# Performance work log

Hardware: AMD Instinct MI355X
Metric: run time of the kernel (lower is better)

## Reference

```python
import math
import jax, jax.numpy as jnp
from jax import lax
import numpy as np

B, SEQ, D_MODEL = 8, 1024, 512
R, K, H = 3, 3, 4
DE, DH, DU, DTR, DCONV, DEMB = 64, 64, 32, 4, 3, 10


def setup_inputs() -> dict:
    key = jax.random.key(0)
    ks = iter(jax.random.split(key, 48))
    def nrm(shape, s=0.05):
        return jax.random.normal(next(ks), shape, jnp.float32) * s
    inp = {}
    inp['x'] = jax.random.normal(next(ks), (B, SEQ, D_MODEL), jnp.float32)
    # Mamba params, leading dims (R, 2) = (layer, fwd/bwd direction)
    inp['m_in_w'] = nrm((R, 2, D_MODEL, 2 * DE))
    inp['m_conv_w'] = nrm((R, 2, DE, DCONV), 0.2)
    inp['m_conv_b'] = nrm((R, 2, DE), 0.1)
    inp['m_xproj_w'] = nrm((R, 2, DE, DTR + 2 * DH))
    inp['m_dt_w'] = nrm((R, 2, DTR, DE), 0.2)
    inp['m_dt_b'] = nrm((R, 2, DE), 0.1)
    inp['m_Alog'] = jnp.broadcast_to(jnp.log(jnp.arange(1, DH + 1, dtype=jnp.float32)), (R, 2, DE, DH)) + jnp.zeros((R, 2, DE, DH), jnp.float32)
    inp['m_D'] = jnp.ones((R, 2, DE), jnp.float32)
    inp['m_out_w'] = nrm((R, 2, DE, D_MODEL))
    # LayerNorm / FFN params per layer
    inp['ln1_g'] = jnp.ones((R, D_MODEL), jnp.float32)
    inp['ln1_b'] = jnp.zeros((R, D_MODEL), jnp.float32)
    inp['ffn_w1'] = nrm((R, D_MODEL, DU))
    inp['ffn_b1'] = jnp.zeros((R, DU), jnp.float32)
    inp['ffn_w2'] = nrm((R, DU, D_MODEL))
    inp['ffn_b2'] = jnp.zeros((R, D_MODEL), jnp.float32)
    inp['ln2_g'] = jnp.ones((R, D_MODEL), jnp.float32)
    inp['ln2_b'] = jnp.zeros((R, D_MODEL), jnp.float32)
    # MAGAC params (N = D_MODEL nodes, in_dim = SEQ)
    inp['psi_emb'] = jax.random.normal(next(ks), (D_MODEL, DEMB), jnp.float32)
    inp['psi'] = jnp.array(1.0, jnp.float32)
    inp['W_q'] = jax.random.normal(next(ks), (DEMB, H, DEMB), jnp.float32)
    inp['W_k'] = jax.random.normal(next(ks), (DEMB, H, DEMB), jnp.float32)
    inp['attn_alpha'] = jnp.array(0.5, jnp.float32)
    inp['F_w'] = nrm((H, DEMB, K + 1, SEQ))
    inp['f_b'] = jax.random.normal(next(ks), (H, DEMB), jnp.float32)
    inp['head_mix'] = jnp.ones((H,), jnp.float32)
    inp['head_w'] = nrm((D_MODEL,))
    inp['head_b'] = jnp.zeros((), jnp.float32)
    return inp


def _layernorm(x, g, b, eps=1e-5):
    mu = x.mean(-1, keepdims=True)
    v = ((x - mu) ** 2).mean(-1, keepdims=True)
    return (x - mu) / jnp.sqrt(v + eps) * g + b


def _mamba(x, in_w, conv_w, conv_b, xproj_w, dt_w, dt_b, Alog, Dp, out_w):
    b, l, _ = x.shape
    xr = x @ in_w                              # (b,l,2*DE)
    xp, res = jnp.split(xr, 2, axis=-1)
    # depthwise causal conv (torch pads k-1 both sides then truncates to l == left-pad k-1)
    xc = xp.transpose(0, 2, 1)                 # (b,DE,l)
    xc = lax.conv_general_dilated(xc, conv_w[:, None, :], (1,), [(DCONV - 1, 0)],
                                  feature_group_count=DE,
                                  dimension_numbers=('NCH', 'OIH', 'NCH'))
    xc = xc + conv_b[None, :, None]
    xp = jax.nn.silu(xc.transpose(0, 2, 1))    # (b,l,DE)
    A = -jnp.exp(Alog)                         # (DE,DH)
    x_dbl = xp @ xproj_w                       # (b,l,DTR+2*DH)
    delta = jax.nn.softplus(x_dbl[..., :DTR] @ dt_w + dt_b)   # (b,l,DE)
    Bm = x_dbl[..., DTR:DTR + DH]
    Cm = x_dbl[..., DTR + DH:]
    dA = jnp.exp(delta[..., None] * A)                         # (b,l,DE,DH)
    dBu = delta[..., None] * Bm[:, :, None, :] * xp[..., None] # (b,l,DE,DH)
    def step(s, inp):
        dAt, dBt, ct = inp
        s = dAt * s + dBt
        return s, jnp.einsum('bdn,bn->bd', s, ct)
    s0 = jnp.zeros((b, DE, DH), x.dtype)
    _, ys = lax.scan(step, s0, (dA.transpose(1, 0, 2, 3), dBu.transpose(1, 0, 2, 3), Cm.transpose(1, 0, 2)))
    y = ys.transpose(1, 0, 2) + xp * Dp
    y = y * jax.nn.sigmoid(res)
    return y @ out_w


def _magac(xg, psi_emb, psi, W_q, W_k, attn_alpha, F_w, f_b, head_mix):
    # xg: (B, N, L); eval-mode deterministic path
    diff = psi_emb[:, None, :] - psi_emb[None, :, :]
    A_base = jax.nn.softmax(jnp.exp(-psi * (diff ** 2).sum(-1)), axis=1)   # (N,N)
    Q = jnp.einsum('nd,dhm->nhm', psi_emb, W_q)
    Kq = jnp.einsum('nd,dhm->nhm', psi_emb, W_k)
    attn = jax.nn.softmax(jnp.einsum('nhd,mhd->hnm', Q, Kq) / math.sqrt(DEMB), axis=-1)
    alpha = jax.nn.sigmoid(attn_alpha)
    A_eff = alpha * A_base[None] + (1.0 - alpha) * attn                    # (H,N,N)
    N = psi_emb.shape[0]
    I = jnp.broadcast_to(jnp.eye(N, dtype=xg.dtype), (H, N, N))
    sup = [I, A_eff]
    for _ in range(K - 1):
        sup.append(2.0 * jnp.matmul(A_eff, sup[-1]) - sup[-2])             # Chebyshev
    sup = jnp.stack(sup, axis=1)                                           # (H,K+1,N,N)
    Wf = jnp.einsum('nd,hdkl->hnkl', psi_emb, F_w)                         # (H,N,K+1,L)
    bf = jnp.einsum('nd,hd->hn', psi_emb, f_b)                             # (H,N)
    x_g = jnp.einsum('hknm,bml->bhknl', sup, xg)                           # (B,H,K+1,N,L)
    out_h = jnp.einsum('bhknl,hnkl->bhn', x_g, Wf) + bf[None]
    mix = jax.nn.softmax(head_mix)
    return jnp.einsum('bhn,h->bn', out_h, mix)


def reference(x, m_in_w, m_conv_w, m_conv_b, m_xproj_w, m_dt_w, m_dt_b, m_Alog, m_D, m_out_w,
              ln1_g, ln1_b, ffn_w1, ffn_b1, ffn_w2, ffn_b2, ln2_g, ln2_b,
              psi_emb, psi, W_q, W_k, attn_alpha, F_w, f_b, head_mix, head_w, head_b):
    for i in range(R):
        mf = (m_in_w[i, 0], m_conv_w[i, 0], m_conv_b[i, 0], m_xproj_w[i, 0], m_dt_w[i, 0],
              m_dt_b[i, 0], m_Alog[i, 0], m_D[i, 0], m_out_w[i, 0])
        mb = (m_in_w[i, 1], m_conv_w[i, 1], m_conv_b[i, 1], m_xproj_w[i, 1], m_dt_w[i, 1],
              m_dt_b[i, 1], m_Alog[i, 1], m_D[i, 1], m_out_w[i, 1])
        y_f = _mamba(x, *mf)
        y_b = jnp.flip(_mamba(jnp.flip(x, 1), *mb), 1)
        y = _layernorm(x + y_f + y_b, ln1_g[i], ln1_b[i])
        z = jax.nn.relu(y @ ffn_w1[i] + ffn_b1[i]) @ ffn_w2[i] + ffn_b2[i]
        x = _layernorm(y + z, ln2_g[i], ln2_b[i])
    g = _magac(x.transpose(0, 2, 1), psi_emb, psi, W_q, W_k, attn_alpha, F_w, f_b, head_mix)
    # eval-mode Bayesian MC: all mc_eval samples identical -> mean=g, var=1e-6
    log_var_node = jnp.full_like(g, jnp.log(jnp.asarray(1e-6, g.dtype)))
    mu = g @ head_w + head_b
    var = jnp.exp(log_var_node) @ (head_w ** 2) + 1e-6
    return mu, jnp.log(var)
```

## Files before the change

### kernel.cpp

```cpp
#include <hip/hip_runtime.h>
#include <math.h>

#define SEQL 1024
#define NB 8
#define DMOD 512

__device__ __forceinline__ float blk_sum4(float v, volatile float* sb) {
#pragma unroll
  for (int off = 32; off; off >>= 1) v += __shfl_xor(v, off, 64);
  int lid = threadIdx.x & 63, wid = threadIdx.x >> 6;
  if (lid == 0) sb[wid] = v;
  __syncthreads();
  float t = sb[0] + sb[1] + sb[2] + sb[3];
  __syncthreads();
  return t;
}
__device__ __forceinline__ float blk_max4(float v, volatile float* sb) {
#pragma unroll
  for (int off = 32; off; off >>= 1) v = fmaxf(v, __shfl_xor(v, off, 64));
  int lid = threadIdx.x & 63, wid = threadIdx.x >> 6;
  if (lid == 0) sb[wid] = v;
  __syncthreads();
  float t = fmaxf(fmaxf(sb[0], sb[1]), fmaxf(sb[2], sb[3]));
  __syncthreads();
  return t;
}

__global__ __launch_bounds__(256) void gemm_f32(
    const float* __restrict__ A, long aStr,
    const float* __restrict__ B, long bStr,
    const float* __restrict__ Dm, long dStr,
    float* __restrict__ C, long cStr, long cChunkStr,
    int M, int N, int K, int lda, int ldb, int ldd, int ldc,
    float alpha, float beta, int kchunks) {
  __shared__ float As[2][16][68];
  __shared__ float Bs[2][16][64];
  const int zz = blockIdx.z;
  const int zb = zz / kchunks, kc = zz % kchunks;
  A += (long)zb * aStr + (long)kc * K;
  B += (long)zb * bStr + (long)kc * K * ldb;
  Dm += (long)zb * dStr;
  C += (long)zb * cStr + (long)kc * cChunkStr;
  const int tid = threadIdx.x;
  const int m0 = blockIdx.y * 64, n0 = blockIdx.x * 64;
  const int tx = tid & 15, ty = tid >> 4;
  const int arow = tid >> 2, acol = (tid & 3) << 2;
  const int brow = tid >> 4, bcol = (tid & 15) << 2;
  const bool aOk = (m0 + arow < M);
  const float* Aptr = A + (long)(m0 + arow) * lda + acol;
  const float* Bptr = B + (long)brow * ldb;
  const int bc = n0 + bcol;
  const int kIters = K >> 4;
  float acc[4][4] = {};

  auto loadB = [&](int it) {
    const float* Bk = Bptr + (long)it * 16 * ldb;
    float4 r;
    if (bc + 3 < N) r = *(const float4*)(Bk + bc);
    else {
      r.x = (bc + 0 < N) ? Bk[bc + 0] : 0.f;
      r.y = (bc + 1 < N) ? Bk[bc + 1] : 0.f;
      r.z = (bc + 2 < N) ? Bk[bc + 2] : 0.f;
      r.w = (bc + 3 < N) ? Bk[bc + 3] : 0.f;
    }
    return r;
  };

  float4 av = make_float4(0.f, 0.f, 0.f, 0.f);
  if (aOk) av = *(const float4*)(Aptr);
  float4 bv = loadB(0);
  As[0][acol + 0][arow] = av.x; As[0][acol + 1][arow] = av.y;
  As[0][acol + 2][arow] = av.z; As[0][acol + 3][arow] = av.w;
  *(float4*)&Bs[0][brow][bcol] = bv;

  for (int it = 0; it < kIters; ++it) {
    const int cur = it & 1;
    __syncthreads();
    const bool more = (it + 1 < kIters);
    if (more) {
      if (aOk) av = *(const float4*)(Aptr + (it + 1) * 16);
      bv = loadB(it + 1);
    }
#pragma unroll
    for (int kk = 0; kk < 16; ++kk) {
      float4 aq = *(const float4*)&As[cur][kk][ty << 2];
      float4 bq = *(const float4*)&Bs[cur][kk][tx << 2];
      float aa[4] = {aq.x, aq.y, aq.z, aq.w};
      float bb[4] = {bq.x, bq.y, bq.z, bq.w};
#pragma unroll
      for (int i = 0; i < 4; ++i)
#pragma unroll
        for (int j = 0; j < 4; ++j) acc[i][j] = fmaf(aa[i], bb[j], acc[i][j]);
    }
    if (more) {
      const int nxt = cur ^ 1;
      As[nxt][acol + 0][arow] = av.x; As[nxt][acol + 1][arow] = av.y;
      As[nxt][acol + 2][arow] = av.z; As[nxt][acol + 3][arow] = av.w;
      *(float4*)&Bs[nxt][brow][bcol] = bv;
    }
  }
#pragma unroll
  for (int i = 0; i < 4; ++i) {
    int row = m0 + (ty << 2) + i;
    if (row >= M) continue;
#pragma unroll
    for (int j = 0; j < 4; ++j) {
      int col = n0 + (tx << 2) + j;
      if (col >= N) continue;
      float v = alpha * acc[i][j];
      if (beta != 0.f) v += beta * Dm[(long)row * ldd + col];
      C[(long)row * ldc + col] = v;
    }
  }
}

__global__ __launch_bounds__(256) void convproj(
    const float* __restrict__ xr, const float* __restrict__ cw,
    const float* __restrict__ cb, const float* __restrict__ pw,
    const float* __restrict__ dw, const float* __restrict__ db,
    float* __restrict__ Bm, float* __restrict__ Cm,
    float* __restrict__ xpT, float* __restrict__ dlT, float* __restrict__ sigT) {
  int dir = blockIdx.y;
  int L = blockIdx.x;
  int r = L & 7, q = L >> 3;
  int blk = r * 256 + q;
  int wv = threadIdx.x >> 6, e = threadIdx.x & 63;
  int tok = blk * 4 + wv;
  int b = tok >> 10, t = tok & 1023;
  const float* xrp = xr + (long)dir * 1048576;
  long rb = (long)tok * 128;
  const float* w = cw + dir * 192;
  float w0 = w[e * 3 + 0], w1 = w[e * 3 + 1], w2 = w[e * 3 + 2];
  float acc = cb[dir * 64 + e] + w2 * xrp[rb + e];
  if (dir == 0) {
    if (t >= 1) acc += w1 * xrp[rb - 128 + e];
    if (t >= 2) acc += w0 * xrp[rb - 256 + e];
  } else {
    if (t <= 1022) acc += w1 * xrp[rb + 128 + e];
    if (t <= 1021) acc += w0 * xrp[rb + 256 + e];
  }
  float xpv = acc / (1.f + __expf(-acc));
  float res = xrp[rb + 64 + e];
  float sg = 1.f / (1.f + __expf(-res));
  long tidx = (long)dir * 524288 + (long)b * 65536 + (long)e * 1024 + t;
  xpT[tidx] = xpv;
  sigT[tidx] = sg;
  const float* wp = pw + dir * 8448;
  float aB = 0.f, aC = 0.f, aD = 0.f;
#pragma unroll
  for (int k = 0; k < 64; ++k) {
    float xk = __shfl(xpv, k, 64);
    const float* wr = wp + k * 132;
    aB = fmaf(xk, wr[4 + e], aB);
    aC = fmaf(xk, wr[68 + e], aC);
    aD = fmaf(xk, wr[e & 3], aD);
  }
  long ob = (long)dir * 524288 + (long)tok * 64;
  Bm[ob + e] = aB;
  Cm[ob + e] = aC;
  const float* dwp = dw + dir * 256;
  float dv = db[dir * 64 + e];
#pragma unroll
  for (int rr = 0; rr < 4; ++rr) dv = fmaf(__shfl(aD, rr, 64), dwp[rr * 64 + e], dv);
  dlT[tidx] = fmaxf(dv, 0.f) + log1pf(__expf(-fabsf(dv)));
}

__device__ __forceinline__ void remap16w(int wv, int& d, int& b, int& dir, int& c) {
  int L = blockIdx.x + 64 * (blockIdx.y + 8 * blockIdx.z);
  int r = L & 7, q = L >> 3;
  d = q & 63;
  int U = (q >> 6) * 8 + r;
  int cq = U & 3;
  dir = (U >> 2) & 1;
  b = U >> 3;
  c = cq * 4 + wv;
}

__global__ __launch_bounds__(256) void scan_p1(
    const float* __restrict__ dlT, const float* __restrict__ xpT,
    const float* __restrict__ Bm, const float* __restrict__ Alog,
    float* __restrict__ Aprod, float* __restrict__ Send) {
  int wv = threadIdx.x >> 6, n = threadIdx.x & 63;
  int d, b, dir, c;
  remap16w(wv, d, b, dir, c);
  long tbase = (long)dir * 524288 + (long)b * 65536 + (long)d * 1024;
  int t0 = c * 64;
  float dl, u;
  if (dir == 0) {
    dl = dlT[tbase + t0 + n];
    u = xpT[tbase + t0 + n] * dl;
  } else {
    dl = dlT[tbase + 1023 - t0 - n];
    u = xpT[tbase + 1023 - t0 - n] * dl;
  }
  float a_dn = -__expf(Alog[dir * 4096 + d * 64 + n]);
  int tg0 = dir ? (1023 - t0) : t0;
  long bstep = dir ? -64 : 64;
  const float* bp = Bm + (long)dir * 524288 + ((long)b * 1024 + tg0) * 64 + n;
  float s = 0.f, ap = 1.f;
#pragma unroll
  for (int st = 0; st < 64; ++st) {
    float bt = *bp; bp += bstep;
    float dlv = __shfl(dl, st, 64);
    float uu = __shfl(u, st, 64);
    float a = __expf(dlv * a_dn);
    ap *= a;
    s = fmaf(a, s, uu * bt);
  }
  long sidx = ((long)((dir * 8 + b) * 64 + d)) * 1024 + c * 64 + n;
  Aprod[sidx] = ap;
  Send[sidx] = s;
}

__global__ __launch_bounds__(64) void scan_p2(
    const float* __restrict__ Aprod, const float* __restrict__ Send,
    float* __restrict__ Sin) {
  int d = blockIdx.x, b = blockIdx.y, dir = blockIdx.z;
  int n = threadIdx.x;
  long base = ((long)((dir * 8 + b) * 64 + d)) * 1024;
  float s = 0.f;
#pragma unroll
  for (int c = 0; c < 16; ++c) {
    Sin[base + c * 64 + n] = s;
    s = fmaf(Aprod[base + c * 64 + n], s, Send[base + c * 64 + n]);
  }
}

__global__ __launch_bounds__(256) void scan_p3(
    const float* __restrict__ dlT, const float* __restrict__ xpT,
    const float* __restrict__ sigT, const float* __restrict__ Bm,
    const float* __restrict__ Cm, const float* __restrict__ Alog,
    const float* __restrict__ Dp, const float* __restrict__ Sin,
    float* __restrict__ ycat) {
  __shared__ float sP[4][16 * 65];
  int wv = threadIdx.x >> 6, n = threadIdx.x & 63;
  int d, b, dir, c;
  remap16w(wv, d, b, dir, c);
  long tbase = (long)dir * 524288 + (long)b * 65536 + (long)d * 1024;
  int t0 = c * 64;
  float dl, xp, sg;
  if (dir == 0) {
    dl = dlT[tbase + t0 + n];
    xp = xpT[tbase + t0 + n];
    sg = sigT[tbase + t0 + n];
  } else {
    dl = dlT[tbase + 1023 - t0 - n];
    xp = xpT[tbase + 1023 - t0 - n];
    sg = sigT[tbase + 1023 - t0 - n];
  }
  float u = xp * dl;
  float a_dn = -__expf(Alog[dir * 4096 + d * 64 + n]);
  float dpd = Dp[dir * 64 + d];
  int tg0 = dir ? (1023 - t0) : t0;
  long bstep = dir ? -64 : 64;
  long boff = (long)dir * 524288 + ((long)b * 1024 + tg0) * 64 + n;
  const float* bp = Bm + boff;
  const float* cp = Cm + boff;
  long sidx = ((long)((dir * 8 + b) * 64 + d)) * 1024 + c * 64 + n;
  float s = Sin[sidx];
  int r4 = n >> 2, q4 = n & 3;
  for (int ph = 0; ph < 4; ++ph) {
#pragma unroll
    for (int k = 0; k < 16; ++k) {
      int st = ph * 16 + k;
      float bt = *bp; bp += bstep;
      float ct = *cp; cp += bstep;
      float dlv = __shfl(dl, st, 64);
      float uu = __shfl(u, st, 64);
      float a = __expf(dlv * a_dn);
      s = fmaf(a, s, uu * bt);
      sP[wv][k * 65 + n] = s * ct;
    }
    __syncthreads();
    float p = 0.f;
#pragma unroll
    for (int k = 0; k < 16; ++k) p += sP[wv][r4 * 65 + q4 * 16 + k];
    p += __shfl_xor(p, 1, 64);
    p += __shfl_xor(p, 2, 64);
    int stl = ph * 16 + r4;
    float xpv_r = __shfl(xp, stl, 64);
    float sgv = __shfl(sg, stl, 64);
    if (q4 == 0) {
      int tl = t0 + stl;
      int tg = dir ? 1023 - tl : tl;
      ycat[((long)b * 1024 + tg) * 128 + dir * 64 + d] = (p + xpv_r * dpd) * sgv;
    }
    __syncthreads();
  }
}

__global__ __launch_bounds__(256) void ln_ffn_ln(
    float* __restrict__ x, const float* __restrict__ g1, const float* __restrict__ b1v,
    const float* __restrict__ w1, const float* __restrict__ bb1,
    const float* __restrict__ w2, const float* __restrict__ bb2,
    const float* __restrict__ g2, const float* __restrict__ b2v) {
  __shared__ float ybuf[2][512];
  __shared__ float rbuf[2][256];
  __shared__ float zbuf[2][32];
  __shared__ float red4[16];
  int tid = threadIdx.x;
  int lid = tid & 63, wid = tid >> 6;
  float* row0 = x + (long)blockIdx.x * 1024;
  float* row1 = row0 + 512;
  float a0 = row0[tid], b0 = row0[tid + 256];
  float a1 = row1[tid], b1 = row1[tid + 256];
  float s0 = a0 + b0, q0 = a0 * a0 + b0 * b0;
  float s1 = a1 + b1, q1 = a1 * a1 + b1 * b1;
#pragma unroll
  for (int off = 32; off; off >>= 1) {
    s0 += __shfl_xor(s0, off, 64); q0 += __shfl_xor(q0, off, 64);
    s1 += __shfl_xor(s1, off, 64); q1 += __shfl_xor(q1, off, 64);
  }
  if (lid == 0) {
    red4[wid * 4 + 0] = s0; red4[wid * 4 + 1] = q0;
    red4[wid * 4 + 2] = s1; red4[wid * 4 + 3] = q1;
  }
  __syncthreads();
  float S0 = red4[0] + red4[4] + red4[8] + red4[12];
  float Q0 = red4[1] + red4[5] + red4[9] + red4[13];
  float S1 = red4[2] + red4[6] + red4[10] + red4[14];
  float Q1 = red4[3] + red4[7] + red4[11] + red4[15];
  float mu0 = S0 * (1.f / 512.f), mu1 = S1 * (1.f / 512.f);
  float r0 = 1.f / sqrtf(Q0 * (1.f / 512.f) - mu0 * mu0 + 1e-5f);
  float r1 = 1.f / sqrtf(Q1 * (1.f / 512.f) - mu1 * mu1 + 1e-5f);
  float g1a = g1[tid], g1b = g1[tid + 256];
  float b1a = b1v[tid], b1b = b1v[tid + 256];
  float y0a = (a0 - mu0) * r0 * g1a + b1a;
  float y0b = (b0 - mu0) * r0 * g1b + b1b;
  float y1a = (a1 - mu1) * r1 * g1a + b1a;
  float y1b = (b1 - mu1) * r1 * g1b + b1b;
  ybuf[0][tid] = y0a; ybuf[0][tid + 256] = y0b;
  ybuf[1][tid] = y1a; ybuf[1][tid + 256] = y1b;
  __syncthreads();
  int u = tid & 31, seg = tid >> 5;
  int k0 = seg * 64;
  float p0 = 0.f, p1 = 0.f;
#pragma unroll
  for (int k = 0; k < 64; k += 4) {
    float4 ya = *(const float4*)&ybuf[0][k0 + k];
    float4 yb = *(const float4*)&ybuf[1][k0 + k];
    float w1v0 = w1[(k0 + k + 0) * 32 + u];
    float w1v1 = w1[(k0 + k + 1) * 32 + u];
    float w1v2 = w1[(k0 + k + 2) * 32 + u];
    float w1v3 = w1[(k0 + k + 3) * 32 + u];
    p0 = fmaf(ya.w, w1v3, fmaf(ya.z, w1v2, fmaf(ya.y, w1v1, fmaf(ya.x, w1v0, p0))));
    p1 = fmaf(yb.w, w1v3, fmaf(yb.z, w1v2, fmaf(yb.y, w1v1, fmaf(yb.x, w1v0, p1))));
  }
  rbuf[0][seg * 32 + u] = p0;
  rbuf[1][seg * 32 + u] = p1;
  __syncthreads();
  if (tid < 64) {
    int t = tid >> 5, uu = tid & 31;
    float zv = bb1[uu];
#pragma unroll
    for (int sg = 0; sg < 8; ++sg) zv += rbuf[t][sg * 32 + uu];
    zbuf[t][uu] = fmaxf(zv, 0.f);
  }
  __syncthreads();
  float bb2a = bb2[tid], bb2b = bb2[tid + 256];
  float h0a = y0a + bb2a, h0b = y0b + bb2b;
  float h1a = y1a + bb2a, h1b = y1b + bb2b;
#pragma unroll
  for (int uu = 0; uu < 32; ++uu) {
    float wa = w2[uu * 512 + tid], wb = w2[uu * 512 + tid + 256];
    float z0 = zbuf[0][uu], z1 = zbuf[1][uu];
    h0a = fmaf(z0, wa, h0a); h1a = fmaf(z1, wa, h1a);
    h0b = fmaf(z0, wb, h0b); h1b = fmaf(z1, wb, h1b);
  }
  s0 = h0a + h0b; q0 = h0a * h0a + h0b * h0b;
  s1 = h1a + h1b; q1 = h1a * h1a + h1b * h1b;
#pragma unroll
  for (int off = 32; off; off >>= 1) {
    s0 += __shfl_xor(s0, off, 64); q0 += __shfl_xor(q0, off, 64);
    s1 += __shfl_xor(s1, off, 64); q1 += __shfl_xor(q1, off, 64);
  }
  __syncthreads();
  if (lid == 0) {
    red4[wid * 4 + 0] = s0; red4[wid * 4 + 1] = q0;
    red4[wid * 4 + 2] = s1; red4[wid * 4 + 3] = q1;
  }
  __syncthreads();
  S0 = red4[0] + red4[4] + red4[8] + red4[12];
  Q0 = red4[1] + red4[5] + red4[9] + red4[13];
  S1 = red4[2] + red4[6] + red4[10] + red4[14];
  Q1 = red4[3] + red4[7] + red4[11] + red4[15];
  mu0 = S0 * (1.f / 512.f); mu1 = S1 * (1.f / 512.f);
  r0 = 1.f / sqrtf(Q0 * (1.f / 512.f) - mu0 * mu0 + 1e-5f);
  r1 = 1.f / sqrtf(Q1 * (1.f / 512.f) - mu1 * mu1 + 1e-5f);
  float g2a = g2[tid], g2b = g2[tid + 256];
  float b2a = b2v[tid], b2b = b2v[tid + 256];
  row0[tid] = (h0a - mu0) * r0 * g2a + b2a;
  row0[tid + 256] = (h0b - mu0) * r0 * g2b + b2b;
  row1[tid] = (h1a - mu1) * r1 * g2a + b2a;
  row1[tid + 256] = (h1b - mu1) * r1 * g2b + b2b;
}

__global__ __launch_bounds__(64) void qk_kernel(
    const float* __restrict__ e, const float* __restrict__ Wq,
    const float* __restrict__ Wk, float* __restrict__ Qb, float* __restrict__ Kb) {
  int n = blockIdx.x, j = threadIdx.x;
  __shared__ float en[10];
  if (j < 10) en[j] = e[n * 10 + j];
  __syncthreads();
  if (j < 40) {
    float q = 0.f, k = 0.f;
#pragma unroll
    for (int dd = 0; dd < 10; ++dd) {
      q = fmaf(en[dd], Wq[dd * 40 + j], q);
      k = fmaf(en[dd], Wk[dd * 40 + j], k);
    }
    Qb[n * 40 + j] = q;
    Kb[n * 40 + j] = k;
  }
}

__global__ __launch_bounds__(256) void aeff_kernel(
    const float* __restrict__ e, const float* __restrict__ Qb,
    const float* __restrict__ Kb, const float* __restrict__ psi_p,
    const float* __restrict__ alpha_p, float* __restrict__ Aef) {
  int n = blockIdx.x, h = blockIdx.y, tid = threadIdx.x;
  __shared__ float s_at[512];
  __shared__ float s_bs[512];
  __shared__ float qn[10];
  __shared__ float en[10];
  __shared__ float red[4];
  if (tid < 10) { qn[tid] = Qb[n * 40 + h * 10 + tid]; en[tid] = e[n * 10 + tid]; }
  __syncthreads();
  float psi = psi_p[0];
  float alpha = 1.f / (1.f + __expf(-alpha_p[0]));
  const float isq = 0.3162277660168379f;
  for (int m = tid; m < 512; m += 256) {
    float sc = 0.f, d2 = 0.f;
#pragma unroll
    for (int dd = 0; dd < 10; ++dd) {
      sc = fmaf(qn[dd], Kb[m * 40 + h * 10 + dd], sc);
      float df = en[dd] - e[m * 10 + dd];
      d2 = fmaf(df, df, d2);
    }
    s_at[m] = sc * isq;
    s_bs[m] = __expf(-psi * d2);
  }
  __syncthreads();
  float m1 = -1e30f, m2 = -1e30f;
  for (int m = tid; m < 512; m += 256) { m1 = fmaxf(m1, s_at[m]); m2 = fmaxf(m2, s_bs[m]); }
  m1 = blk_max4(m1, red);
  m2 = blk_max4(m2, red);
  float e1 = 0.f, e2 = 0.f;
  for (int m = tid; m < 512; m += 256) {
    float a = __expf(s_at[m] - m1); s_at[m] = a; e1 += a;
    float bq = __expf(s_bs[m] - m2); s_bs[m] = bq; e2 += bq;
  }
  e1 = blk_sum4(e1, red);
  e2 = blk_sum4(e2, red);
  float r1 = (1.f - alpha) / e1, r2 = alpha / e2;
  float* outp = Aef + (long)h * 262144 + (long)n * 512;
  for (int m = tid; m < 512; m += 256) outp[m] = r2 * s_bs[m] + r1 * s_at[m];
}

__global__ void xpose_kernel(const float* __restrict__ DbufP,
                             float* __restrict__ X3, float* __restrict__ X2s,
                             float* __restrict__ X13, float* __restrict__ X02) {
  int idx = blockIdx.x * 256 + threadIdx.x;
  if (idx >= 163840) return;
  int c = idx % 80;
  int m = (idx / 80) % 512;
  int h = idx / 40960;
  int d = c >> 3, b = c & 7;
  long base = (long)(b * 160 + h * 40 + d * 4) * 512 + m;
  float k0 = 0.f, k1 = 0.f, k2 = 0.f, k3 = 0.f;
#pragma unroll
  for (int p = 0; p < 4; ++p) {
    const float* Dp_ = DbufP + (long)p * 655360;
    k0 += Dp_[base];
    k1 += Dp_[base + 512];
    k2 += Dp_[base + 1024];
    k3 += Dp_[base + 1536];
  }
  X3[idx] = k3;
  X2s[idx] = k2;
  X13[idx] = k1 - 3.f * k3;
  X02[idx] = k0 - k2;
}

__global__ void outh_kernel(const float* __restrict__ e, const float* __restrict__ fb,
                            const float* __restrict__ Zt, const float* __restrict__ hm,
                            float* __restrict__ g) {
  int idx = blockIdx.x * 256 + threadIdx.x;
  if (idx >= 4096) return;
  int n = idx & 511, b = idx >> 9;
  float h0 = hm[0], h1 = hm[1], h2 = hm[2], h3 = hm[3];
  float mx = fmaxf(fmaxf(h0, h1), fmaxf(h2, h3));
  float x0 = __expf(h0 - mx), x1 = __expf(h1 - mx), x2 = __expf(h2 - mx), x3 = __expf(h3 - mx);
  float es = x0 + x1 + x2 + x3;
  float mixv[4] = {x0 / es, x1 / es, x2 / es, x3 / es};
  float acc = 0.f;
  for (int h = 0; h < 4; ++h) {
    float oh = 0.f;
#pragma unroll
    for (int dd = 0; dd < 10; ++dd) {
      float ev = e[n * 10 + dd];
      float v = Zt[((long)h * 512 + n) * 80 + dd * 8 + b] + fb[h * 10 + dd];
      oh = fmaf(ev, v, oh);
    }
    acc = fmaf(mixv[h], oh, acc);
  }
  g[b * 512 + n] = acc;
}

__global__ __launch_bounds__(256) void head_kernel(
    const float* __restrict__ g, const float* __restrict__ hw,
    const float* __restrict__ hb, float* __restrict__ out) {
  __shared__ float red[4];
  int b = blockIdx.x, tid = threadIdx.x;
  float w0 = hw[tid], w1 = hw[tid + 256];
  float v = g[b * 512 + tid] * w0 + g[b * 512 + tid + 256] * w1;
  float q = w0 * w0 + w1 * w1;
  float mu = blk_sum4(v, red);
  float s2 = blk_sum4(q, red);
  if (tid == 0) {
    out[b] = mu + hb[0];
    out[8 + b] = logf(1e-6f * s2 + 1e-6f);
  }
}

extern "C" void kernel_launch(void* const* d_in, const int* in_sizes, int n_in,
                              void* d_out, int out_size, void* d_ws, size_t ws_size,
                              hipStream_t stream) {
  (void)in_sizes; (void)n_in; (void)out_size; (void)ws_size;
  const float* x0    = (const float*)d_in[0];
  const float* in_w  = (const float*)d_in[1];
  const float* cw    = (const float*)d_in[2];
  const float* cb    = (const float*)d_in[3];
  const float* pw    = (const float*)d_in[4];
  const float* dtw   = (const float*)d_in[5];
  const float* dtb   = (const float*)d_in[6];
  const float* Alog  = (const float*)d_in[7];
  const float* Dpar  = (const float*)d_in[8];
  const float* ow    = (const float*)d_in[9];
  const float* l1g   = (const float*)d_in[10];
  const float* l1b   = (const float*)d_in[11];
  const float* fw1   = (const float*)d_in[12];
  const float* fb1   = (const float*)d_in[13];
  const float* fw2   = (const float*)d_in[14];
  const float* fb2   = (const float*)d_in[15];
  const float* l2g   = (const float*)d_in[16];
  const float* l2b   = (const float*)d_in[17];
  const float* emb   = (const float*)d_in[18];
  const float* psi   = (const float*)d_in[19];
  const float* Wq    = (const float*)d_in[20];
  const float* Wk    = (const float*)d_in[21];
  const float* aal   = (const float*)d_in[22];
  const float* Fw    = (const float*)d_in[23];
  const float* fbv   = (const float*)d_in[24];
  const float* hmix  = (const float*)d_in[25];
  const float* hw    = (const float*)d_in[26];
  const float* hb    = (const float*)d_in[27];
  float* out = (float*)d_out;

  float* ws = (float*)d_ws;
  float* xA   = ws;
  float* xB   = xA + 4194304;
  float* scr  = xB + 4194304;
  float* xr   = scr;
  float* Bm   = xr + 2097152;
  float* Cm   = Bm + 1048576;
  float* xpT  = Cm + 1048576;
  float* dlT  = xpT + 1048576;
  float* sigT = dlT + 1048576;
  float* ycat = sigT + 1048576;
  float* Sin  = ycat + 1048576;
  float* Aprod = xr;
  float* Send  = xr + 1048576;
  float* Qb    = scr;
  float* Kb    = Qb + 20480;
  float* Aef   = Kb + 20480;
  float* DbufP = Aef + 1048576;
  float* X3    = DbufP + 2621440;
  float* X2s   = X3 + 163840;
  float* X13   = X2s + 163840;
  float* X02   = X13 + 163840;
  float* Z2    = X02 + 163840;
  float* Z1    = Z2 + 163840;
  float* Zt    = Z1 + 163840;
  float* gb    = Zt + 163840;

  const float* xin = x0;
  float* bufs[3] = {xA, xB, xA};
  for (int i = 0; i < 3; ++i) {
    float* xout = bufs[i];
    gemm_f32<<<dim3(2, 128, 2), 256, 0, stream>>>(
        xin, 0, in_w + (long)i * 131072, 65536, xin, 0, xr, 1048576, 0,
        8192, 128, 512, 512, 128, 0, 128, 1.f, 0.f, 1);
    convproj<<<dim3(2048, 2), 256, 0, stream>>>(
        xr, cw + i * 384, cb + i * 128, pw + i * 16896, dtw + i * 512,
        dtb + i * 128, Bm, Cm, xpT, dlT, sigT);
    scan_p1<<<dim3(64, 8, 8), 256, 0, stream>>>(
        dlT, xpT, Bm, Alog + i * 8192, Aprod, Send);
    scan_p2<<<dim3(64, 8, 2), 64, 0, stream>>>(Aprod, Send, Sin);
    scan_p3<<<dim3(64, 8, 8), 256, 0, stream>>>(
        dlT, xpT, sigT, Bm, Cm, Alog + i * 8192, Dpar + i * 128, Sin, ycat);
    gemm_f32<<<dim3(8, 128, 1), 256, 0, stream>>>(
        ycat, 0, ow + (long)i * 65536, 0, xin, 0, xout, 0, 0,
        8192, 512, 128, 128, 512, 512, 512, 1.f, 1.f, 1);
    ln_ffn_ln<<<4096, 256, 0, stream>>>(
        xout, l1g + i * 512, l1b + i * 512, fw1 + i * 16384, fb1 + i * 32,
        fw2 + i * 16384, fb2 + i * 512, l2g + i * 512, l2b + i * 512);
    xin = xout;
  }
  qk_kernel<<<512, 64, 0, stream>>>(emb, Wq, Wk, Qb, Kb);
  aeff_kernel<<<dim3(512, 4), 256, 0, stream>>>(emb, Qb, Kb, psi, aal, Aef);
  gemm_f32<<<dim3(8, 3, 32), 256, 0, stream>>>(
      Fw, 0, xA, 524288, Fw, 0, DbufP, 81920, 655360,
      160, 512, 256, 1024, 512, 0, 512, 1.f, 0.f, 4);
  xpose_kernel<<<640, 256, 0, stream>>>(DbufP, X3, X2s, X13, X02);
  gemm_f32<<<dim3(2, 8, 4), 256, 0, stream>>>(
      Aef, 262144, X3, 40960, X2s, 40960, Z2, 40960, 0,
      512, 80, 512, 512, 80, 80, 80, 4.f, 2.f, 1);
  gemm_f32<<<dim3(2, 8, 4), 256, 0, stream>>>(
      Aef, 262144, Z2, 40960, X13, 40960, Z1, 40960, 0,
      512, 80, 512, 512, 80, 80, 80, 1.f, 1.f, 1);
  gemm_f32<<<dim3(2, 8, 4), 256, 0, stream>>>(
      Aef, 262144, Z1, 40960, X02, 40960, Zt, 40960, 0,
      512, 80, 512, 512, 80, 80, 80, 1.f, 1.f, 1);
  outh_kernel<<<16, 256, 0, stream>>>(emb, fbv, Zt, hmix, gb);
  head_kernel<<<8, 256, 0, stream>>>(gb, hw, hb, out);
}
```

Measured before the change: 755.8 us.

## Run selective-scan chunks as single-wave blocks and prefetch per-step inputs

The chunked scan kernels now launch one 64-thread wave per block instead of four waves sharing a block, with a new block-to-(batch, direction, chunk, channel) mapping. Instead of shuffling dt and u across lanes each step, every lane loads 16 timesteps of dt and x into registers ahead of the recurrence, and B/C loads are issued per 16-step batch. The per-step shuffles and the four-wave block barrier in scan_p3 go away, and the product of decay factors is split into two chains. scan_p2 also loads all its chunk values before running the serial combine. The cost is more register pressure and redundant broadcast-style loads of dt and x, where every lane reads the same address.

```diff
diff --git a/kernel.cpp b/kernel.cpp
--- a/kernel.cpp
+++ b/kernel.cpp
@@ -165,50 +165,53 @@
   dlT[tidx] = fmaxf(dv, 0.f) + log1pf(__expf(-fabsf(dv)));
 }
 
-__device__ __forceinline__ void remap16w(int wv, int& d, int& b, int& dir, int& c) {
+__device__ __forceinline__ void scan_remap(int& d, int& b, int& dir, int& c) {
   int L = blockIdx.x + 64 * (blockIdx.y + 8 * blockIdx.z);
   int r = L & 7, q = L >> 3;
   d = q & 63;
-  int U = (q >> 6) * 8 + r;
-  int cq = U & 3;
-  dir = (U >> 2) & 1;
-  b = U >> 3;
-  c = cq * 4 + wv;
-}
-
-__global__ __launch_bounds__(256) void scan_p1(
+  int T = (q >> 6) * 8 + r;
+  b = T >> 5;
+  dir = (T >> 4) & 1;
+  c = T & 15;
+}
+
+__global__ __launch_bounds__(64) void scan_p1(
     const float* __restrict__ dlT, const float* __restrict__ xpT,
     const float* __restrict__ Bm, const float* __restrict__ Alog,
     float* __restrict__ Aprod, float* __restrict__ Send) {
-  int wv = threadIdx.x >> 6, n = threadIdx.x & 63;
   int d, b, dir, c;
-  remap16w(wv, d, b, dir, c);
+  scan_remap(d, b, dir, c);
+  int n = threadIdx.x;
   long tbase = (long)dir * 524288 + (long)b * 65536 + (long)d * 1024;
   int t0 = c * 64;
-  float dl, u;
-  if (dir == 0) {
-    dl = dlT[tbase + t0 + n];
-    u = xpT[tbase + t0 + n] * dl;
-  } else {
-    dl = dlT[tbase + 1023 - t0 - n];
-    u = xpT[tbase + 1023 - t0 - n] * dl;
-  }
   float a_dn = -__expf(Alog[dir * 4096 + d * 64 + n]);
   int tg0 = dir ? (1023 - t0) : t0;
   long bstep = dir ? -64 : 64;
   const float* bp = Bm + (long)dir * 524288 + ((long)b * 1024 + tg0) * 64 + n;
-  float s = 0.f, ap = 1.f;
-#pragma unroll
-  for (int st = 0; st < 64; ++st) {
-    float bt = *bp; bp += bstep;
-    float dlv = __shfl(dl, st, 64);
-    float uu = __shfl(u, st, 64);
-    float a = __expf(dlv * a_dn);
-    ap *= a;
-    s = fmaf(a, s, uu * bt);
+  const float* dlrow = dlT + tbase;
+  const float* xprow = xpT + tbase;
+  float s = 0.f, ap0 = 1.f, ap1 = 1.f;
+  for (int sb = 0; sb < 4; ++sb) {
+    float sa[16], su[16];
+#pragma unroll
+    for (int k = 0; k < 16; ++k) {
+      int tl = t0 + sb * 16 + k;
+      int tg = dir ? 1023 - tl : tl;
+      float dv = dlrow[tg];
+      sa[k] = dv;
+      su[k] = dv * xprow[tg];
+    }
+#pragma unroll
+    for (int k = 0; k < 16; ++k) {
+      float bt = bp[(long)k * bstep];
+      float a = __expf(sa[k] * a_dn);
+      if (k & 1) ap1 *= a; else ap0 *= a;
+      s = fmaf(a, s, su[k] * bt);
+    }
+    bp += 16 * bstep;
   }
   long sidx = ((long)((dir * 8 + b) * 64 + d)) * 1024 + c * 64 + n;
-  Aprod[sidx] = ap;
+  Aprod[sidx] = ap0 * ap1;
   Send[sidx] = s;
 }
 
@@ -218,37 +221,36 @@
   int d = blockIdx.x, b = blockIdx.y, dir = blockIdx.z;
   int n = threadIdx.x;
   long base = ((long)((dir * 8 + b) * 64 + d)) * 1024;
+  float apv[16], sev[16];
+#pragma unroll
+  for (int c = 0; c < 16; ++c) {
+    apv[c] = Aprod[base + c * 64 + n];
+    sev[c] = Send[base + c * 64 + n];
+  }
   float s = 0.f;
 #pragma unroll
   for (int c = 0; c < 16; ++c) {
     Sin[base + c * 64 + n] = s;
-    s = fmaf(Aprod[base + c * 64 + n], s, Send[base + c * 64 + n]);
-  }
-}
-
-__global__ __launch_bounds__(256) void scan_p3(
+    s = fmaf(apv[c], s, sev[c]);
+  }
+}
+
+__global__ __launch_bounds__(64) void scan_p3(
     const float* __restrict__ dlT, const float* __restrict__ xpT,
     const float* __restrict__ sigT, const float* __restrict__ Bm,
     const float* __restrict__ Cm, const float* __restrict__ Alog,
     const float* __restrict__ Dp, const float* __restrict__ Sin,
     float* __restrict__ ycat) {
-  __shared__ float sP[4][16 * 65];
-  int wv = threadIdx.x >> 6, n = threadIdx.x & 63;
+  __shared__ float sP[16 * 65];
   int d, b, dir, c;
-  remap16w(wv, d, b, dir, c);
+  scan_remap(d, b, dir, c);
+  int n = threadIdx.x;
   long tbase = (long)dir * 524288 + (long)b * 65536 + (long)d * 1024;
   int t0 = c * 64;
-  float dl, xp, sg;
-  if (dir == 0) {
-    dl = dlT[tbase + t0 + n];
-    xp = xpT[tbase + t0 + n];
-    sg = sigT[tbase + t0 + n];
-  } else {
-    dl = dlT[tbase + 1023 - t0 - n];
-    xp = xpT[tbase + 1023 - t0 - n];
-    sg = sigT[tbase + 1023 - t0 - n];
-  }
-  float u = xp * dl;
+  int tln = t0 + n;
+  int tgn = dir ? 1023 - tln : tln;
+  float xp_l = xpT[tbase + tgn];
+  float sg_l = sigT[tbase + tgn];
   float a_dn = -__expf(Alog[dir * 4096 + d * 64 + n]);
   float dpd = Dp[dir * 64 + d];
   int tg0 = dir ? (1023 - t0) : t0;
@@ -259,27 +261,36 @@
   long sidx = ((long)((dir * 8 + b) * 64 + d)) * 1024 + c * 64 + n;
   float s = Sin[sidx];
   int r4 = n >> 2, q4 = n & 3;
+  const float* dlrow = dlT + tbase;
+  const float* xprow = xpT + tbase;
   for (int ph = 0; ph < 4; ++ph) {
+    float sa[16], su[16];
 #pragma unroll
     for (int k = 0; k < 16; ++k) {
-      int st = ph * 16 + k;
-      float bt = *bp; bp += bstep;
-      float ct = *cp; cp += bstep;
-      float dlv = __shfl(dl, st, 64);
-      float uu = __shfl(u, st, 64);
-      float a = __expf(dlv * a_dn);
-      s = fmaf(a, s, uu * bt);
-      sP[wv][k * 65 + n] = s * ct;
-    }
+      int tl = t0 + ph * 16 + k;
+      int tg = dir ? 1023 - tl : tl;
+      float dv = dlrow[tg];
+      sa[k] = dv;
+      su[k] = dv * xprow[tg];
+    }
+#pragma unroll
+    for (int k = 0; k < 16; ++k) {
+      float bt = bp[(long)k * bstep];
+      float ct = cp[(long)k * bstep];
+      float a = __expf(sa[k] * a_dn);
+      s = fmaf(a, s, su[k] * bt);
+      sP[k * 65 + n] = s * ct;
+    }
+    bp += 16 * bstep; cp += 16 * bstep;
     __syncthreads();
     float p = 0.f;
 #pragma unroll
-    for (int k = 0; k < 16; ++k) p += sP[wv][r4 * 65 + q4 * 16 + k];
+    for (int k = 0; k < 16; ++k) p += sP[r4 * 65 + q4 * 16 + k];
     p += __shfl_xor(p, 1, 64);
     p += __shfl_xor(p, 2, 64);
     int stl = ph * 16 + r4;
-    float xpv_r = __shfl(xp, stl, 64);
-    float sgv = __shfl(sg, stl, 64);
+    float xpv_r = __shfl(xp_l, stl, 64);
+    float sgv = __shfl(sg_l, stl, 64);
     if (q4 == 0) {
       int tl = t0 + stl;
       int tg = dir ? 1023 - tl : tl;
@@ -594,10 +605,10 @@
     convproj<<<dim3(2048, 2), 256, 0, stream>>>(
         xr, cw + i * 384, cb + i * 128, pw + i * 16896, dtw + i * 512,
         dtb + i * 128, Bm, Cm, xpT, dlT, sigT);
-    scan_p1<<<dim3(64, 8, 8), 256, 0, stream>>>(
+    scan_p1<<<dim3(64, 8, 32), 64, 0, stream>>>(
         dlT, xpT, Bm, Alog + i * 8192, Aprod, Send);
     scan_p2<<<dim3(64, 8, 2), 64, 0, stream>>>(Aprod, Send, Sin);
-    scan_p3<<<dim3(64, 8, 8), 256, 0, stream>>>(
+    scan_p3<<<dim3(64, 8, 32), 64, 0, stream>>>(
         dlT, xpT, sigT, Bm, Cm, Alog + i * 8192, Dpar + i * 128, Sin, ycat);
     gemm_f32<<<dim3(8, 128, 1), 256, 0, stream>>>(
         ycat, 0, ow + (long)i * 65536, 0, xin, 0, xout, 0, 0,
```

Result: slower. 772.0 us (+2.1%).
